# Optimization experiments

Hardware: AMD Instinct MI355X
Metric: run time of the kernel (lower is better)

Reference implementation:

```python
import jax, jax.numpy as jnp
import numpy as np

ENC_H = 512
DEC_H = 512
FIELD = 128

def setup_inputs() -> dict:
    key = jax.random.key(0)
    ks = jax.random.split(key, 12)
    B, S, T = 8, 256, 32
    def lin(k, fan_in, fan_out):
        k1, k2 = jax.random.split(k)
        bound = 1.0 / np.sqrt(fan_in)
        W = jax.random.uniform(k1, (fan_in, fan_out), minval=-bound, maxval=bound, dtype=jnp.float32)
        b = jax.random.uniform(k2, (fan_out,), minval=-bound, maxval=bound, dtype=jnp.float32)
        return W, b
    W1, b1 = lin(ks[0], ENC_H, DEC_H)
    W2, b2 = lin(ks[1], DEC_H, DEC_H)
    W3, b3 = lin(ks[2], FIELD, DEC_H)
    W4, b4 = lin(ks[3], DEC_H, DEC_H)
    return {
        "output": jax.random.normal(ks[4], (B, T, DEC_H), dtype=jnp.float32),
        "encoder_hidden": jax.random.normal(ks[5], (S, B, ENC_H), dtype=jnp.float32),
        "input_z": jax.random.normal(ks[6], (B, S, FIELD), dtype=jnp.float32),
        "W1": W1, "b1": b1, "W2": W2, "b2": b2,
        "W3": W3, "b3": b3, "W4": W4, "b4": b4,
    }

def reference(output, encoder_hidden, input_z, W1, b1, W2, b2, W3, b3, W4, b4):
    S, B, He = encoder_hidden.shape
    # tanh(lin1(encoder_hidden)) then .view(B, S, D)  (reshape, NOT transpose -- faithful to torch .view)
    out_hs = jnp.tanh(encoder_hidden @ W1 + b1).reshape(B, S, -1)      # [B,S,D]
    enc_h = encoder_hidden.reshape(B, S, He)                            # [B,S,He]
    out_fds = jnp.tanh(input_z @ W3 + b3)                               # [B,S,D]
    out2 = jnp.tanh(output @ W2 + b2)                                   # [B,T,D]
    out3 = jnp.tanh(output @ W4 + b4)                                   # [B,T,D]
    # vectorized over timesteps: g1[b,s,t,d] = out_hs[b,s,d]*out2[b,t,d]
    g1 = out_hs[:, :, None, :] * out2[:, None, :, :]                    # [B,S,T,D]
    alpha = jax.nn.softmax(g1, axis=1)                                  # softmax over S, per feature d
    g2 = out_fds[:, :, None, :] * out3[:, None, :, :]                   # [B,S,T,D]
    beta = jax.nn.softmax(g2, axis=1)
    q = alpha * beta                                                    # [B,S,T,D]
    qn = jax.lax.stop_gradient(jnp.sum(q, axis=1, keepdims=True))       # detached normalizer
    gamma = q / qn                                                      # [B,S,T,D]
    contex = jnp.sum(gamma * enc_h[:, :, None, :], axis=1)              # [B,T,D]
    concat_vectors = jnp.concatenate([output, contex], axis=-1)         # [B,T,2D]
    # attn: list over t of gamma[:, :, t, :] -> stacked [B,T,S,D]
    attn = jnp.transpose(gamma, (0, 2, 1, 3))
    return (concat_vectors, attn)
```

## Files before the change

kernel.cpp:

```cpp
#include <hip/hip_runtime.h>


typedef __attribute__((ext_vector_type(8))) short bf16x8;
typedef __attribute__((ext_vector_type(4))) float f32x4;

__device__ __forceinline__ unsigned short f2bf(float x) {
    union { float f; unsigned u; } v; v.f = x;
    unsigned r = v.u + 0x7fffu + ((v.u >> 16) & 1u);
    return (unsigned short)(r >> 16);
}

__global__ __launch_bounds__(256) void cvt_all_k(
    const float* __restrict__ E, const float* __restrict__ Z, const float* __restrict__ O,
    unsigned short* __restrict__ Ebf, unsigned short* __restrict__ Zbf, unsigned short* __restrict__ Obf)
{
    int b = blockIdx.x;
    const float* src; unsigned short* dst; int base;
    if (b < 1024)      { src = E; dst = Ebf; base = b; }
    else if (b < 1280) { src = Z; dst = Zbf; base = b - 1024; }
    else               { src = O; dst = Obf; base = b - 1280; }
    int i = base * 1024 + threadIdx.x * 4;
    float4 v = *(const float4*)(src + i);
    ushort4 r;
    r.x = f2bf(v.x); r.y = f2bf(v.y); r.z = f2bf(v.z); r.w = f2bf(v.w);
    *(ushort4*)(dst + i) = r;
}

__global__ __launch_bounds__(256) void transpose_all_k(
    const float* __restrict__ W1, const float* __restrict__ W2,
    const float* __restrict__ W3, const float* __restrict__ W4,
    unsigned short* __restrict__ W1T, unsigned short* __restrict__ W2T,
    unsigned short* __restrict__ W3T, unsigned short* __restrict__ W4T)
{
    const float* W; unsigned short* WT; int K;
    switch (blockIdx.z) {
      case 0:  W = W1; WT = W1T; K = 512; break;
      case 1:  W = W2; WT = W2T; K = 512; break;
      case 2:  W = W3; WT = W3T; K = 128; break;
      default: W = W4; WT = W4T; K = 512; break;
    }
    int k0 = blockIdx.y * 32;
    if (k0 >= K) return;
    int n0 = blockIdx.x * 32;
    __shared__ float tile[32][33];
    int tx = threadIdx.x, ty = threadIdx.y;
    #pragma unroll
    for (int i = 0; i < 32; i += 8)
        tile[ty + i][tx] = W[(k0 + ty + i) * 512 + n0 + tx];
    __syncthreads();
    #pragma unroll
    for (int i = 0; i < 32; i += 8)
        WT[(n0 + ty + i) * K + k0 + tx] = f2bf(tile[tx][ty + i]);
}

__global__ __launch_bounds__(256) void gemm_all_k(
    const unsigned short* __restrict__ Ebf, const unsigned short* __restrict__ Zbf,
    const unsigned short* __restrict__ Obf,
    const unsigned short* __restrict__ W1T, const unsigned short* __restrict__ W3T,
    const unsigned short* __restrict__ W2T, const unsigned short* __restrict__ W4T,
    const float* __restrict__ b1, const float* __restrict__ b3,
    const float* __restrict__ b2, const float* __restrict__ b4,
    float* __restrict__ L1, float* __restrict__ F,
    float* __restrict__ O2, float* __restrict__ O3)
{
    const unsigned short* A; const unsigned short* BT; const float* bias; float* C;
    int M, K;
    switch (blockIdx.z) {
      case 0:  A = Ebf; BT = W1T; bias = b1; C = L1; M = 2048; K = 512; break;
      case 1:  A = Zbf; BT = W3T; bias = b3; C = F;  M = 2048; K = 128; break;
      case 2:  A = Obf; BT = W2T; bias = b2; C = O2; M = 256;  K = 512; break;
      default: A = Obf; BT = W4T; bias = b4; C = O3; M = 256;  K = 512; break;
    }
    int m0 = blockIdx.x * 64;
    if (m0 >= M) return;
    int n0 = blockIdx.y * 64;

    __shared__ unsigned short As[64 * 40];
    __shared__ unsigned short Bs[64 * 40];

    int tid  = threadIdx.x;
    int wave = tid >> 6;
    int lane = tid & 63;
    int lm   = lane & 15;
    int lq   = lane >> 4;

    int srow = tid >> 2;
    int scol = (tid & 3) * 8;

    f32x4 acc[4];
    #pragma unroll
    for (int c = 0; c < 4; ++c) acc[c] = f32x4{0.f, 0.f, 0.f, 0.f};

    for (int k0 = 0; k0 < K; k0 += 32) {
        __syncthreads();
        *(uint4*)(&As[srow * 40 + scol]) = *(const uint4*)(&A[(m0 + srow) * K + k0 + scol]);
        *(uint4*)(&Bs[srow * 40 + scol]) = *(const uint4*)(&BT[(n0 + srow) * K + k0 + scol]);
        __syncthreads();
        bf16x8 af = *(const bf16x8*)(&As[(wave * 16 + lm) * 40 + lq * 8]);
        #pragma unroll
        for (int c = 0; c < 4; ++c) {
            bf16x8 bfr = *(const bf16x8*)(&Bs[(c * 16 + lm) * 40 + lq * 8]);
            acc[c] = __builtin_amdgcn_mfma_f32_16x16x32_bf16(af, bfr, acc[c], 0, 0, 0);
        }
    }

    #pragma unroll
    for (int c = 0; c < 4; ++c) {
        int col = n0 + c * 16 + lm;
        float bv = bias[col];
        #pragma unroll
        for (int r = 0; r < 4; ++r) {
            int row = m0 + wave * 16 + lq * 4 + r;
            float x = acc[c][r] + bv;
            x = fminf(fmaxf(x, -15.f), 15.f);
            float t = __expf(2.0f * x);
            C[row * 512 + col] = (t - 1.0f) / (t + 1.0f);
        }
    }
}

__global__ __launch_bounds__(256) void attn_partial_k(
    const float* __restrict__ L1, const float* __restrict__ F,
    const float* __restrict__ O2, const float* __restrict__ O3,
    const float* __restrict__ Enc,
    float* __restrict__ sum_p, float* __restrict__ csum_p)
{
    int b  = blockIdx.x >> 3;
    int sc = blockIdx.x & 7;
    int tc = blockIdx.y;
    int dc = blockIdx.z;
    int d  = dc * 256 + threadIdx.x;

    float c2[16], c3[16], sum[16], csum[16];
    #pragma unroll
    for (int i = 0; i < 16; ++i) {
        int bt = b * 32 + tc * 16 + i;
        c2[i] = O2[bt * 512 + d];
        c3[i] = O3[bt * 512 + d];
        sum[i] = 0.f; csum[i] = 0.f;
    }

    int s0 = sc * 32;
    const float* L1b = L1  + (b * 256 + s0) * 512 + d;
    const float* Fb  = F   + (b * 256 + s0) * 512 + d;
    const float* Eb  = Enc + (b * 256 + s0) * 512 + d;

    #pragma unroll 2
    for (int s = 0; s < 32; ++s) {
        float l1 = L1b[s * 512];
        float f  = Fb[s * 512];
        float eh = Eb[s * 512];
        #pragma unroll
        for (int i = 0; i < 16; ++i) {
            float e = __expf(l1 * c2[i] + f * c3[i]);
            sum[i]  += e;
            csum[i] += e * eh;
        }
    }

    #pragma unroll
    for (int i = 0; i < 16; ++i) {
        int idx = ((b * 8 + sc) * 32 + tc * 16 + i) * 512 + d;
        sum_p[idx]  = sum[i];
        csum_p[idx] = csum[i];
    }
}

__global__ __launch_bounds__(256) void attn_finalize_k(
    const float* __restrict__ sum_p, const float* __restrict__ csum_p,
    const float* __restrict__ Out,
    float* __restrict__ out0, float* __restrict__ invA)
{
    int bt = blockIdx.x;
    int d  = blockIdx.y * 256 + threadIdx.x;
    int b  = bt >> 5, t = bt & 31;

    float sum = 0.f, csum = 0.f;
    #pragma unroll
    for (int sc = 0; sc < 8; ++sc) {
        int idx = ((b * 8 + sc) * 32 + t) * 512 + d;
        sum  += sum_p[idx];
        csum += csum_p[idx];
    }
    float inv = 1.0f / sum;
    invA[bt * 512 + d] = inv;
    out0[bt * 1024 + d]       = Out[bt * 512 + d];
    out0[bt * 1024 + 512 + d] = csum * inv;
}

__global__ __launch_bounds__(256) void attn_write_k(
    const float* __restrict__ L1, const float* __restrict__ F,
    const float* __restrict__ O2, const float* __restrict__ O3,
    const float* __restrict__ invA,
    float* __restrict__ attn)
{
    int b  = blockIdx.x;
    int s0 = blockIdx.y * 4 + ((threadIdx.x >> 7) * 2);
    int d4 = (threadIdx.x & 127) * 4;

    float4 l1[2], f[2];
    #pragma unroll
    for (int j = 0; j < 2; ++j) {
        l1[j] = *(const float4*)(L1 + (b * 256 + s0 + j) * 512 + d4);
        f[j]  = *(const float4*)(F  + (b * 256 + s0 + j) * 512 + d4);
    }

    for (int t = 0; t < 32; ++t) {
        int bt = b * 32 + t;
        float4 c2 = *(const float4*)(O2   + bt * 512 + d4);
        float4 c3 = *(const float4*)(O3   + bt * 512 + d4);
        float4 iv = *(const float4*)(invA + bt * 512 + d4);
        #pragma unroll
        for (int j = 0; j < 2; ++j) {
            float4 g;
            g.x = __expf(l1[j].x * c2.x + f[j].x * c3.x) * iv.x;
            g.y = __expf(l1[j].y * c2.y + f[j].y * c3.y) * iv.y;
            g.z = __expf(l1[j].z * c2.z + f[j].z * c3.z) * iv.z;
            g.w = __expf(l1[j].w * c2.w + f[j].w * c3.w) * iv.w;
            *(float4*)(attn + ((size_t)(bt * 256 + s0 + j)) * 512 + d4) = g;
        }
    }
}

extern "C" void kernel_launch(void* const* d_in, const int* in_sizes, int n_in,
                              void* d_out, int out_size, void* d_ws, size_t ws_size,
                              hipStream_t stream)
{
    const float* Out = (const float*)d_in[0];
    const float* Enc = (const float*)d_in[1];
    const float* Z   = (const float*)d_in[2];
    const float* W1  = (const float*)d_in[3];
    const float* b1  = (const float*)d_in[4];
    const float* W2  = (const float*)d_in[5];
    const float* b2  = (const float*)d_in[6];
    const float* W3  = (const float*)d_in[7];
    const float* b3  = (const float*)d_in[8];
    const float* W4  = (const float*)d_in[9];
    const float* b4  = (const float*)d_in[10];

    char* ws = (char*)d_ws;
    size_t off = 0;
    auto alloc = [&](size_t n) -> char* {
        char* p = ws + off; off += (n + 255) & ~(size_t)255; return p;
    };
    unsigned short* Ebf = (unsigned short*)alloc(1048576 * 2);
    unsigned short* Zbf = (unsigned short*)alloc(262144 * 2);
    unsigned short* Obf = (unsigned short*)alloc(131072 * 2);
    unsigned short* W1T = (unsigned short*)alloc(262144 * 2);
    unsigned short* W2T = (unsigned short*)alloc(262144 * 2);
    unsigned short* W3T = (unsigned short*)alloc(65536 * 2);
    unsigned short* W4T = (unsigned short*)alloc(262144 * 2);
    float* L1    = (float*)alloc(1048576 * 4);
    float* F     = (float*)alloc(1048576 * 4);
    float* O2    = (float*)alloc(131072 * 4);
    float* O3    = (float*)alloc(131072 * 4);
    float* sum_p = (float*)alloc(1048576 * 4);
    float* csum_p= (float*)alloc(1048576 * 4);
    float* invA  = (float*)alloc(131072 * 4);

    float* out0 = (float*)d_out;
    float* attn = out0 + 262144;

    hipLaunchKernelGGL(cvt_all_k, dim3(1408), dim3(256), 0, stream,
                       Enc, Z, Out, Ebf, Zbf, Obf);
    hipLaunchKernelGGL(transpose_all_k, dim3(16, 16, 4), dim3(32, 8), 0, stream,
                       W1, W2, W3, W4, W1T, W2T, W3T, W4T);
    hipLaunchKernelGGL(gemm_all_k, dim3(32, 8, 4), dim3(256), 0, stream,
                       Ebf, Zbf, Obf, W1T, W3T, W2T, W4T,
                       b1, b3, b2, b4, L1, F, O2, O3);
    hipLaunchKernelGGL(attn_partial_k, dim3(64, 2, 2), dim3(256), 0, stream,
                       L1, F, O2, O3, Enc, sum_p, csum_p);
    hipLaunchKernelGGL(attn_finalize_k, dim3(256, 2), dim3(256), 0, stream,
                       sum_p, csum_p, Out, out0, invA);
    hipLaunchKernelGGL(attn_write_k, dim3(8, 64), dim3(256), 0, stream,
                       L1, F, O2, O3, invA, attn);
}
```

Measured before the change: 206.6 us.

## Merge prep kernels, compact GEMM grid, widen K tile, rebalance attention grids

Merges the bf16 conversion and weight transpose into one launch and flattens the GEMM grid so no blocks exit early. The GEMM K-step grows to 64 per iteration, halving the synchronisations. The partial attention pass is split into more, smaller blocks (16 S-chunks, 8 timesteps each) for more parallelism, at the cost of twice the partial-sum traffic in finalize. The attn writer handles 4 S rows per thread and uses nontemporal stores for the large output.

```diff
diff --git a/kernel.cpp b/kernel.cpp
--- a/kernel.cpp
+++ b/kernel.cpp
@@ -10,40 +10,38 @@
     return (unsigned short)(r >> 16);
 }
 
-__global__ __launch_bounds__(256) void cvt_all_k(
+__global__ __launch_bounds__(256) void prep_k(
     const float* __restrict__ E, const float* __restrict__ Z, const float* __restrict__ O,
-    unsigned short* __restrict__ Ebf, unsigned short* __restrict__ Zbf, unsigned short* __restrict__ Obf)
-{
-    int b = blockIdx.x;
-    const float* src; unsigned short* dst; int base;
-    if (b < 1024)      { src = E; dst = Ebf; base = b; }
-    else if (b < 1280) { src = Z; dst = Zbf; base = b - 1024; }
-    else               { src = O; dst = Obf; base = b - 1280; }
-    int i = base * 1024 + threadIdx.x * 4;
-    float4 v = *(const float4*)(src + i);
-    ushort4 r;
-    r.x = f2bf(v.x); r.y = f2bf(v.y); r.z = f2bf(v.z); r.w = f2bf(v.w);
-    *(ushort4*)(dst + i) = r;
-}
-
-__global__ __launch_bounds__(256) void transpose_all_k(
     const float* __restrict__ W1, const float* __restrict__ W2,
     const float* __restrict__ W3, const float* __restrict__ W4,
+    unsigned short* __restrict__ Ebf, unsigned short* __restrict__ Zbf,
+    unsigned short* __restrict__ Obf,
     unsigned short* __restrict__ W1T, unsigned short* __restrict__ W2T,
     unsigned short* __restrict__ W3T, unsigned short* __restrict__ W4T)
 {
+    int bid = blockIdx.x;
+    if (bid < 1408) {
+        const float* src; unsigned short* dst; int base;
+        if (bid < 1024)      { src = E; dst = Ebf; base = bid; }
+        else if (bid < 1280) { src = Z; dst = Zbf; base = bid - 1024; }
+        else                 { src = O; dst = Obf; base = bid - 1280; }
+        int i = base * 1024 + threadIdx.x * 4;
+        float4 v = *(const float4*)(src + i);
+        ushort4 r;
+        r.x = f2bf(v.x); r.y = f2bf(v.y); r.z = f2bf(v.z); r.w = f2bf(v.w);
+        *(ushort4*)(dst + i) = r;
+        return;
+    }
+    int tb = bid - 1408;
     const float* W; unsigned short* WT; int K;
-    switch (blockIdx.z) {
-      case 0:  W = W1; WT = W1T; K = 512; break;
-      case 1:  W = W2; WT = W2T; K = 512; break;
-      case 2:  W = W3; WT = W3T; K = 128; break;
-      default: W = W4; WT = W4T; K = 512; break;
-    }
-    int k0 = blockIdx.y * 32;
-    if (k0 >= K) return;
-    int n0 = blockIdx.x * 32;
+    if (tb < 256)      {            W = W1; WT = W1T; K = 512; }
+    else if (tb < 512) { tb -= 256; W = W2; WT = W2T; K = 512; }
+    else if (tb < 576) { tb -= 512; W = W3; WT = W3T; K = 128; }
+    else               { tb -= 576; W = W4; WT = W4T; K = 512; }
+    int n0 = (tb & 15) * 32;
+    int k0 = (tb >> 4) * 32;
     __shared__ float tile[32][33];
-    int tx = threadIdx.x, ty = threadIdx.y;
+    int tx = threadIdx.x & 31, ty = threadIdx.x >> 5;
     #pragma unroll
     for (int i = 0; i < 32; i += 8)
         tile[ty + i][tx] = W[(k0 + ty + i) * 512 + n0 + tx];
@@ -63,20 +61,18 @@
     float* __restrict__ L1, float* __restrict__ F,
     float* __restrict__ O2, float* __restrict__ O3)
 {
+    int id = blockIdx.x;
     const unsigned short* A; const unsigned short* BT; const float* bias; float* C;
-    int M, K;
-    switch (blockIdx.z) {
-      case 0:  A = Ebf; BT = W1T; bias = b1; C = L1; M = 2048; K = 512; break;
-      case 1:  A = Zbf; BT = W3T; bias = b3; C = F;  M = 2048; K = 128; break;
-      case 2:  A = Obf; BT = W2T; bias = b2; C = O2; M = 256;  K = 512; break;
-      default: A = Obf; BT = W4T; bias = b4; C = O3; M = 256;  K = 512; break;
-    }
-    int m0 = blockIdx.x * 64;
-    if (m0 >= M) return;
-    int n0 = blockIdx.y * 64;
-
-    __shared__ unsigned short As[64 * 40];
-    __shared__ unsigned short Bs[64 * 40];
+    int K;
+    if (id < 256)      {             A = Ebf; BT = W1T; bias = b1; C = L1; K = 512; }
+    else if (id < 512) { id -= 256;  A = Zbf; BT = W3T; bias = b3; C = F;  K = 128; }
+    else if (id < 544) { id -= 512;  A = Obf; BT = W2T; bias = b2; C = O2; K = 512; }
+    else               { id -= 544;  A = Obf; BT = W4T; bias = b4; C = O3; K = 512; }
+    int m0 = (id >> 3) * 64;
+    int n0 = (id & 7) * 64;
+
+    __shared__ unsigned short As[64 * 72];
+    __shared__ unsigned short Bs[64 * 72];
 
     int tid  = threadIdx.x;
     int wave = tid >> 6;
@@ -85,22 +81,29 @@
     int lq   = lane >> 4;
 
     int srow = tid >> 2;
-    int scol = (tid & 3) * 8;
+    int scol = (tid & 3) * 16;
 
     f32x4 acc[4];
     #pragma unroll
     for (int c = 0; c < 4; ++c) acc[c] = f32x4{0.f, 0.f, 0.f, 0.f};
 
-    for (int k0 = 0; k0 < K; k0 += 32) {
+    for (int k0 = 0; k0 < K; k0 += 64) {
         __syncthreads();
-        *(uint4*)(&As[srow * 40 + scol]) = *(const uint4*)(&A[(m0 + srow) * K + k0 + scol]);
-        *(uint4*)(&Bs[srow * 40 + scol]) = *(const uint4*)(&BT[(n0 + srow) * K + k0 + scol]);
+        const unsigned short* Ap = &A[(m0 + srow) * K + k0 + scol];
+        const unsigned short* Bp = &BT[(n0 + srow) * K + k0 + scol];
+        *(uint4*)(&As[srow * 72 + scol])     = *(const uint4*)(Ap);
+        *(uint4*)(&As[srow * 72 + scol + 8]) = *(const uint4*)(Ap + 8);
+        *(uint4*)(&Bs[srow * 72 + scol])     = *(const uint4*)(Bp);
+        *(uint4*)(&Bs[srow * 72 + scol + 8]) = *(const uint4*)(Bp + 8);
         __syncthreads();
-        bf16x8 af = *(const bf16x8*)(&As[(wave * 16 + lm) * 40 + lq * 8]);
-        #pragma unroll
-        for (int c = 0; c < 4; ++c) {
-            bf16x8 bfr = *(const bf16x8*)(&Bs[(c * 16 + lm) * 40 + lq * 8]);
-            acc[c] = __builtin_amdgcn_mfma_f32_16x16x32_bf16(af, bfr, acc[c], 0, 0, 0);
+        #pragma unroll
+        for (int ks = 0; ks < 2; ++ks) {
+            bf16x8 af = *(const bf16x8*)(&As[(wave * 16 + lm) * 72 + ks * 32 + lq * 8]);
+            #pragma unroll
+            for (int c = 0; c < 4; ++c) {
+                bf16x8 bfr = *(const bf16x8*)(&Bs[(c * 16 + lm) * 72 + ks * 32 + lq * 8]);
+                acc[c] = __builtin_amdgcn_mfma_f32_16x16x32_bf16(af, bfr, acc[c], 0, 0, 0);
+            }
         }
     }
 
@@ -125,33 +128,32 @@
     const float* __restrict__ Enc,
     float* __restrict__ sum_p, float* __restrict__ csum_p)
 {
-    int b  = blockIdx.x >> 3;
-    int sc = blockIdx.x & 7;
+    int b  = blockIdx.x >> 4;
+    int sc = blockIdx.x & 15;
     int tc = blockIdx.y;
-    int dc = blockIdx.z;
-    int d  = dc * 256 + threadIdx.x;
-
-    float c2[16], c3[16], sum[16], csum[16];
-    #pragma unroll
-    for (int i = 0; i < 16; ++i) {
-        int bt = b * 32 + tc * 16 + i;
+    int d  = blockIdx.z * 256 + threadIdx.x;
+
+    float c2[8], c3[8], sum[8], csum[8];
+    #pragma unroll
+    for (int i = 0; i < 8; ++i) {
+        int bt = b * 32 + tc * 8 + i;
         c2[i] = O2[bt * 512 + d];
         c3[i] = O3[bt * 512 + d];
         sum[i] = 0.f; csum[i] = 0.f;
     }
 
-    int s0 = sc * 32;
+    int s0 = sc * 16;
     const float* L1b = L1  + (b * 256 + s0) * 512 + d;
     const float* Fb  = F   + (b * 256 + s0) * 512 + d;
     const float* Eb  = Enc + (b * 256 + s0) * 512 + d;
 
     #pragma unroll 2
-    for (int s = 0; s < 32; ++s) {
+    for (int s = 0; s < 16; ++s) {
         float l1 = L1b[s * 512];
         float f  = Fb[s * 512];
         float eh = Eb[s * 512];
         #pragma unroll
-        for (int i = 0; i < 16; ++i) {
+        for (int i = 0; i < 8; ++i) {
             float e = __expf(l1 * c2[i] + f * c3[i]);
             sum[i]  += e;
             csum[i] += e * eh;
@@ -159,8 +161,8 @@
     }
 
     #pragma unroll
-    for (int i = 0; i < 16; ++i) {
-        int idx = ((b * 8 + sc) * 32 + tc * 16 + i) * 512 + d;
+    for (int i = 0; i < 8; ++i) {
+        int idx = ((b * 16 + sc) * 32 + tc * 8 + i) * 512 + d;
         sum_p[idx]  = sum[i];
         csum_p[idx] = csum[i];
     }
@@ -177,8 +179,8 @@
 
     float sum = 0.f, csum = 0.f;
     #pragma unroll
-    for (int sc = 0; sc < 8; ++sc) {
-        int idx = ((b * 8 + sc) * 32 + t) * 512 + d;
+    for (int sc = 0; sc < 16; ++sc) {
+        int idx = ((b * 16 + sc) * 32 + t) * 512 + d;
         sum  += sum_p[idx];
         csum += csum_p[idx];
     }
@@ -194,30 +196,31 @@
     const float* __restrict__ invA,
     float* __restrict__ attn)
 {
-    int b  = blockIdx.x;
-    int s0 = blockIdx.y * 4 + ((threadIdx.x >> 7) * 2);
-    int d4 = (threadIdx.x & 127) * 4;
-
-    float4 l1[2], f[2];
-    #pragma unroll
-    for (int j = 0; j < 2; ++j) {
-        l1[j] = *(const float4*)(L1 + (b * 256 + s0 + j) * 512 + d4);
-        f[j]  = *(const float4*)(F  + (b * 256 + s0 + j) * 512 + d4);
+    int b     = blockIdx.x;
+    int sbase = blockIdx.y * 8 + (threadIdx.x >> 7) * 4;
+    int d4    = (threadIdx.x & 127) * 4;
+
+    f32x4 l1[4], f[4];
+    #pragma unroll
+    for (int j = 0; j < 4; ++j) {
+        l1[j] = *(const f32x4*)(L1 + (b * 256 + sbase + j) * 512 + d4);
+        f[j]  = *(const f32x4*)(F  + (b * 256 + sbase + j) * 512 + d4);
     }
 
     for (int t = 0; t < 32; ++t) {
         int bt = b * 32 + t;
-        float4 c2 = *(const float4*)(O2   + bt * 512 + d4);
-        float4 c3 = *(const float4*)(O3   + bt * 512 + d4);
-        float4 iv = *(const float4*)(invA + bt * 512 + d4);
-        #pragma unroll
-        for (int j = 0; j < 2; ++j) {
-            float4 g;
-            g.x = __expf(l1[j].x * c2.x + f[j].x * c3.x) * iv.x;
-            g.y = __expf(l1[j].y * c2.y + f[j].y * c3.y) * iv.y;
-            g.z = __expf(l1[j].z * c2.z + f[j].z * c3.z) * iv.z;
-            g.w = __expf(l1[j].w * c2.w + f[j].w * c3.w) * iv.w;
-            *(float4*)(attn + ((size_t)(bt * 256 + s0 + j)) * 512 + d4) = g;
+        f32x4 c2 = *(const f32x4*)(O2   + bt * 512 + d4);
+        f32x4 c3 = *(const f32x4*)(O3   + bt * 512 + d4);
+        f32x4 iv = *(const f32x4*)(invA + bt * 512 + d4);
+        #pragma unroll
+        for (int j = 0; j < 4; ++j) {
+            f32x4 g;
+            g[0] = __expf(l1[j][0] * c2[0] + f[j][0] * c3[0]) * iv[0];
+            g[1] = __expf(l1[j][1] * c2[1] + f[j][1] * c3[1]) * iv[1];
+            g[2] = __expf(l1[j][2] * c2[2] + f[j][2] * c3[2]) * iv[2];
+            g[3] = __expf(l1[j][3] * c2[3] + f[j][3] * c3[3]) * iv[3];
+            __builtin_nontemporal_store(
+                g, (f32x4*)(attn + ((size_t)(bt * 256 + sbase + j)) * 512 + d4));
         }
     }
 }
@@ -254,24 +257,23 @@
     float* F     = (float*)alloc(1048576 * 4);
     float* O2    = (float*)alloc(131072 * 4);
     float* O3    = (float*)alloc(131072 * 4);
-    float* sum_p = (float*)alloc(1048576 * 4);
-    float* csum_p= (float*)alloc(1048576 * 4);
+    float* sum_p = (float*)alloc(2097152 * 4);
+    float* csum_p= (float*)alloc(2097152 * 4);
     float* invA  = (float*)alloc(131072 * 4);
 
     float* out0 = (float*)d_out;
     float* attn = out0 + 262144;
 
-    hipLaunchKernelGGL(cvt_all_k, dim3(1408), dim3(256), 0, stream,
-                       Enc, Z, Out, Ebf, Zbf, Obf);
-    hipLaunchKernelGGL(transpose_all_k, dim3(16, 16, 4), dim3(32, 8), 0, stream,
-                       W1, W2, W3, W4, W1T, W2T, W3T, W4T);
-    hipLaunchKernelGGL(gemm_all_k, dim3(32, 8, 4), dim3(256), 0, stream,
+    hipLaunchKernelGGL(prep_k, dim3(2240), dim3(256), 0, stream,
+                       Enc, Z, Out, W1, W2, W3, W4,
+                       Ebf, Zbf, Obf, W1T, W2T, W3T, W4T);
+    hipLaunchKernelGGL(gemm_all_k, dim3(576), dim3(256), 0, stream,
                        Ebf, Zbf, Obf, W1T, W3T, W2T, W4T,
                        b1, b3, b2, b4, L1, F, O2, O3);
-    hipLaunchKernelGGL(attn_partial_k, dim3(64, 2, 2), dim3(256), 0, stream,
+    hipLaunchKernelGGL(attn_partial_k, dim3(128, 4, 2), dim3(256), 0, stream,
                        L1, F, O2, O3, Enc, sum_p, csum_p);
     hipLaunchKernelGGL(attn_finalize_k, dim3(256, 2), dim3(256), 0, stream,
                        sum_p, csum_p, Out, out0, invA);
-    hipLaunchKernelGGL(attn_write_k, dim3(8, 64), dim3(256), 0, stream,
+    hipLaunchKernelGGL(attn_write_k, dim3(8, 32), dim3(256), 0, stream,
                        L1, F, O2, O3, invA, attn);
 }
```

Result: no change. 202.6 us (-1.9%).
